# Optimization experiments

Measured on AMD Instinct MI355X. Metric: run time of the kernel, lower is better.

## Reference

```python
import jax, jax.numpy as jnp
import numpy as np


def setup_inputs() -> dict:
    key = jax.random.key(0)
    k1, k2 = jax.random.split(key)
    B, C, h, w = 8, 128, 56, 56
    query_feature = jax.random.normal(k1, (B, C, h, w), dtype=jnp.float32)
    support_feature = jax.random.normal(k2, (B, C, h, w), dtype=jnp.float32)
    return {"query_feature": query_feature, "support_feature": support_feature}


def reference(query_feature, support_feature):
    q, s = query_feature, support_feature
    B, C, h, w = support_feature.shape
    N = h * w
    # torch .view semantics == row-major reshape (NOT a transpose)
    qf = jnp.reshape(query_feature, (B, N, C))      # [B, N, C]
    sf = jnp.reshape(support_feature, (B, C, N))    # [B, C, N]
    batch_adj = jnp.einsum('bnc,bcm->bnm', qf, sf)  # [B, N, N]
    attn = jax.nn.softmax(batch_adj, axis=-1)
    query_logits = jnp.einsum('bnm,bmc->bnc', attn, qf)          # [B, N, C]
    attention_mask = jax.nn.sigmoid(jnp.sum(batch_adj, axis=-1)) # [B, N]
    query_logits = query_logits * attention_mask[..., None]
    sf2 = jnp.reshape(support_feature, (B, N, C))   # another raw view
    support_logits = sf2 * attention_mask[..., None]
    query_logits = jnp.reshape(query_logits, (B, C, h, w))
    support_logits = jnp.reshape(support_logits, (B, C, h, w))
    return (q + query_logits, s + support_logits)
```

## Files before the change

kernel.cpp:

```cpp
#include <hip/hip_runtime.h>
#include <math.h>

#define B_ 8
#define C_ 128
#define N_ 3136
#define MT 64
#define TILES 49
#define SLICES 98
#define QTB 64
#define QTILES 49
#define CS_STRIDE 100

typedef short bf16x8 __attribute__((ext_vector_type(8)));
typedef float f32x4 __attribute__((ext_vector_type(4)));

__device__ __forceinline__ unsigned short f2bf(float f) {
    union { float f; unsigned u; } x; x.f = f;
    return (unsigned short)((x.u + 0x8000u) >> 16);
}

__device__ __forceinline__ unsigned cvtpk(float lo, float hi) {
    unsigned r;
    asm("v_cvt_pk_bf16_f32 %0, %1, %2" : "=v"(r) : "v"(lo), "v"(hi));
    return r;
}

__device__ __forceinline__ void gl_lds16(const void* g, void* l) {
    __builtin_amdgcn_global_load_lds(
        (const __attribute__((address_space(1))) unsigned int*)g,
        (__attribute__((address_space(3))) unsigned int*)l, 16, 0, 0);
}

__global__ __launch_bounds__(256) void colsum_kernel(const float* __restrict__ s,
                                                     float* __restrict__ csum) {
    int blk = blockIdx.x;
    const float* p = s + (size_t)blk * N_;
    float acc = 0.f;
    for (int i = threadIdx.x; i < N_; i += 256) acc += p[i];
#pragma unroll
    for (int off = 32; off > 0; off >>= 1) acc += __shfl_down(acc, off, 64);
    __shared__ float part[4];
    if ((threadIdx.x & 63) == 0) part[threadIdx.x >> 6] = acc;
    __syncthreads();
    if (threadIdx.x == 0) csum[blk] = part[0] + part[1] + part[2] + part[3];
}

__global__ __launch_bounds__(256) void prep_kernel(const float* __restrict__ q,
                                                   const float* __restrict__ s,
                                                   unsigned short* __restrict__ sfT,
                                                   unsigned short* __restrict__ qfT,
                                                   float* __restrict__ csump) {
    __shared__ unsigned short T[4608];
    const int tid = threadIdx.x, bid = blockIdx.x;
    const int b = bid & 7, m0 = (bid >> 3) * 32;
    const int slice = bid >> 3;
    const float* sb = s + (size_t)b * C_ * N_;
    const float* qb = q + (size_t)b * C_ * N_;

    unsigned short (*TA)[132] = (unsigned short (*)[132])T;
#pragma unroll
    for (int st = 0; st < 4; ++st) {
        int idx = st * 256 + tid;
        int c = idx >> 3, m4 = (idx & 7) * 4;
        float4 v = *(const float4*)&sb[(size_t)c * N_ + m0 + m4];
        TA[m4 + 0][c] = f2bf(v.x);
        TA[m4 + 1][c] = f2bf(v.y);
        TA[m4 + 2][c] = f2bf(v.z);
        TA[m4 + 3][c] = f2bf(v.w);
        float ps = (v.x + v.y) + (v.z + v.w);
        ps += __shfl_xor(ps, 1, 8);
        ps += __shfl_xor(ps, 2, 8);
        ps += __shfl_xor(ps, 4, 8);
        if ((tid & 7) == 0) csump[((size_t)b * C_ + c) * CS_STRIDE + slice] = ps;
    }
    __syncthreads();
    {
        unsigned short* dst = sfT + (size_t)b * N_ * C_;
#pragma unroll
        for (int st = 0; st < 2; ++st) {
            int g = st * 256 + tid;
            int mr = g >> 4, p = g & 15;
            int sw = (mr & 15) ^ ((mr >> 1) & 4);
            int lch = p ^ sw;
            const unsigned short* src = &TA[mr][lch * 8];
            ushort4 a = *(const ushort4*)src;
            ushort4 bq = *(const ushort4*)(src + 4);
            uint4 w;
            w.x = a.x | ((unsigned)a.y << 16);   w.y = a.z | ((unsigned)a.w << 16);
            w.z = bq.x | ((unsigned)bq.y << 16); w.w = bq.z | ((unsigned)bq.w << 16);
            *(uint4*)&dst[(size_t)(m0 + mr) * C_ + p * 8] = w;
        }
    }
    __syncthreads();

    unsigned short (*TB)[34] = (unsigned short (*)[34])T;
#pragma unroll
    for (int st = 0; st < 4; ++st) {
        int idx = st * 256 + tid;
        int r = idx >> 5, c4 = (idx & 31) * 4;
        float4 v = *(const float4*)&qb[(size_t)(m0 + r) * C_ + c4];
        TB[c4 + 0][r] = f2bf(v.x);
        TB[c4 + 1][r] = f2bf(v.y);
        TB[c4 + 2][r] = f2bf(v.z);
        TB[c4 + 3][r] = f2bf(v.w);
    }
    __syncthreads();
    {
        unsigned short* dstb = qfT + (size_t)b * N_ * C_;
        const int tile = m0 >> 6, pbase = (m0 & 32) >> 3;
#pragma unroll
        for (int st = 0; st < 2; ++st) {
            int g = st * 256 + tid;
            int pl = g >> 7, c = g & 127;
            const unsigned short* src = &TB[c][pl * 8];
            ushort2 a0 = *(const ushort2*)(src);
            ushort2 a1 = *(const ushort2*)(src + 2);
            ushort2 a2 = *(const ushort2*)(src + 4);
            ushort2 a3 = *(const ushort2*)(src + 6);
            uint4 w;
            w.x = a0.x | ((unsigned)a0.y << 16); w.y = a1.x | ((unsigned)a1.y << 16);
            w.z = a2.x | ((unsigned)a2.y << 16); w.w = a3.x | ((unsigned)a3.y << 16);
            *(uint4*)&dstb[((size_t)tile * 8 + pbase + pl) * (C_ * 8) + c * 8] = w;
        }
    }
}

__global__ __launch_bounds__(256, 2) void fused_full_kernel(
    const float* __restrict__ q, const float* __restrict__ s,
    const float* __restrict__ csump,
    const unsigned short* __restrict__ sfT,
    const unsigned short* __restrict__ qfT,
    float* __restrict__ out0, float* __restrict__ out1) {

    __shared__ __align__(16) unsigned char SM[65536];
    __shared__ float dred[2][QTB];
    __shared__ float mskd[QTB];
    __shared__ float cs[C_];

    unsigned short* Kb = (unsigned short*)SM;
    unsigned short* Vb = (unsigned short*)(SM + 32768);
    float (*Of)[132] = (float (*)[132])SM;

    const int tid = threadIdx.x;
    const int lane = tid & 63;
    const int wave = tid >> 6;
    const int l15 = lane & 15;
    const int quad = lane >> 4;
    const int qs = wave >> 1;
    const int mg = wave & 1;
    const int bid = blockIdx.x;
    const int b = bid & 7;
    const int qt = bid >> 3;
    const int n0 = qt * QTB;

    const float* qb = q + (size_t)b * C_ * N_;
    const unsigned short* sfTb = sfT + (size_t)b * N_ * C_;
    const unsigned short* qfTb = qfT + (size_t)b * N_ * C_;

    const int sig_base = ((l15 >> 2) << 3) + (l15 & 3);

#pragma unroll
    for (int st = 0; st < 4; ++st) {
        int i = st * 256 + tid;
        gl_lds16(sfTb + (size_t)(i >> 4) * C_ + (i & 15) * 8,
                 &Kb[(st * 256 + wave * 64) * 8]);
        gl_lds16(qfTb + (size_t)i * 8,
                 &Vb[(st * 256 + wave * 64) * 8]);
    }

    if (tid < C_) {
        float a = 0.f;
        const float* cp = csump + ((size_t)b * C_ + tid) * CS_STRIDE;
#pragma unroll 7
        for (int sl = 0; sl < SLICES; ++sl) a += cp[sl];
        cs[tid] = a;
    }
    __syncthreads();

    bf16x8 qa[2][4];
    float dotp[2];
#pragma unroll
    for (int rt = 0; rt < 2; ++rt) {
        int grow = n0 + qs * 32 + rt * 16 + l15;
        float dp = 0.f;
#pragma unroll
        for (int ks = 0; ks < 4; ++ks) {
            int c0 = ks * 32 + quad * 8;
            float4 f0 = *(const float4*)&qb[(size_t)grow * C_ + c0];
            float4 f1 = *(const float4*)&qb[(size_t)grow * C_ + c0 + 4];
            dp += f0.x * cs[c0 + 0] + f0.y * cs[c0 + 1] +
                  f0.z * cs[c0 + 2] + f0.w * cs[c0 + 3] +
                  f1.x * cs[c0 + 4] + f1.y * cs[c0 + 5] +
                  f1.z * cs[c0 + 6] + f1.w * cs[c0 + 7];
            union { unsigned w[4]; bf16x8 v; } t;
            t.w[0] = cvtpk(f0.x, f0.y); t.w[1] = cvtpk(f0.z, f0.w);
            t.w[2] = cvtpk(f1.x, f1.y); t.w[3] = cvtpk(f1.z, f1.w);
            qa[rt][ks] = t.v;
        }
        dotp[rt] = dp;
    }
#pragma unroll
    for (int rt = 0; rt < 2; ++rt) {
        float d = dotp[rt];
        d += __shfl_xor(d, 16, 64);
        d += __shfl_xor(d, 32, 64);
        if (mg == 0 && quad == 0) mskd[qs * 32 + rt * 16 + l15] = d;
    }

    f32x4 O[2][8];
#pragma unroll
    for (int rt = 0; rt < 2; ++rt)
#pragma unroll
        for (int nt = 0; nt < 8; ++nt) O[rt][nt] = (f32x4){0.f, 0.f, 0.f, 0.f};
    float dsum[2] = {0.f, 0.f};

    for (int tt = 0; tt < TILES; ++tt) {
        const int cur = tt & 1;

        __builtin_amdgcn_s_barrier();

        if (tt + 1 < TILES) {
            const int nxt = cur ^ 1;
            const size_t m1 = (size_t)(tt + 1) * MT;
#pragma unroll
            for (int st = 0; st < 4; ++st) {
                int i = st * 256 + tid;
                gl_lds16(sfTb + (m1 + (i >> 4)) * C_ + (i & 15) * 8,
                         &Kb[nxt * (MT * C_) + (st * 256 + wave * 64) * 8]);
                gl_lds16(qfTb + (size_t)(tt + 1) * (MT * C_) + (size_t)i * 8,
                         &Vb[nxt * (MT * C_) + (st * 256 + wave * 64) * 8]);
            }
            asm volatile("s_waitcnt vmcnt(8)" ::: "memory");
        } else {
            asm volatile("s_waitcnt vmcnt(0)" ::: "memory");
        }
        __builtin_amdgcn_s_barrier();

        bf16x8 vfr[8];
#pragma unroll
        for (int nt = 0; nt < 8; ++nt)
            vfr[nt] = *(const bf16x8*)&Vb[cur * (MT * C_) + ((mg * 4 + quad) * C_ + nt * 16 + l15) * 8];

        f32x4 acc[2][2];
        __builtin_amdgcn_s_setprio(1);
#pragma unroll
        for (int ct = 0; ct < 2; ++ct) {
            const int mrow = sig_base + (ct << 2);
            const int sw = (mrow & 15) ^ ((mrow >> 1) & 4);
            const int row = mg * 32 + mrow;
            acc[ct][0] = (f32x4){0.f, 0.f, 0.f, 0.f};
            acc[ct][1] = (f32x4){0.f, 0.f, 0.f, 0.f};
#pragma unroll
            for (int ks = 0; ks < 4; ++ks) {
                int ch = (ks * 4 + quad) ^ sw;
                bf16x8 af = *(const bf16x8*)&Kb[cur * (MT * C_) + row * C_ + ch * 8];
                acc[ct][0] = __builtin_amdgcn_mfma_f32_16x16x32_bf16(af, qa[0][ks], acc[ct][0], 0, 0, 0);
                acc[ct][1] = __builtin_amdgcn_mfma_f32_16x16x32_bf16(af, qa[1][ks], acc[ct][1], 0, 0, 0);
            }
        }
        __builtin_amdgcn_s_setprio(0);

        bf16x8 pa[2];
#pragma unroll
        for (int rt = 0; rt < 2; ++rt) {
            float e0 = __expf(acc[0][rt][0]);
            float e1 = __expf(acc[0][rt][1]);
            float e2 = __expf(acc[0][rt][2]);
            float e3 = __expf(acc[0][rt][3]);
            float e4 = __expf(acc[1][rt][0]);
            float e5 = __expf(acc[1][rt][1]);
            float e6 = __expf(acc[1][rt][2]);
            float e7 = __expf(acc[1][rt][3]);
            dsum[rt] += ((e0 + e1) + (e2 + e3)) + ((e4 + e5) + (e6 + e7));
            union { unsigned w[4]; bf16x8 v; } pk;
            pk.w[0] = cvtpk(e0, e1); pk.w[1] = cvtpk(e2, e3);
            pk.w[2] = cvtpk(e4, e5); pk.w[3] = cvtpk(e6, e7);
            pa[rt] = pk.v;
        }

        __builtin_amdgcn_s_setprio(1);
#pragma unroll
        for (int nt = 0; nt < 8; ++nt) {
            O[0][nt] = __builtin_amdgcn_mfma_f32_16x16x32_bf16(pa[0], vfr[nt], O[0][nt], 0, 0, 0);
            O[1][nt] = __builtin_amdgcn_mfma_f32_16x16x32_bf16(pa[1], vfr[nt], O[1][nt], 0, 0, 0);
        }
        __builtin_amdgcn_s_setprio(0);
    }

#pragma unroll
    for (int rt = 0; rt < 2; ++rt) {
        float d = dsum[rt];
        d += __shfl_xor(d, 16, 64);
        d += __shfl_xor(d, 32, 64);
        if (quad == 0) dred[mg][qs * 32 + rt * 16 + l15] = d;
    }

    __syncthreads();

    if (mg == 1) {
#pragma unroll
        for (int rt = 0; rt < 2; ++rt)
#pragma unroll
            for (int nt = 0; nt < 8; ++nt)
#pragma unroll
                for (int r = 0; r < 4; ++r)
                    Of[qs * 32 + rt * 16 + quad * 4 + r][nt * 16 + l15] = O[rt][nt][r];
    }
    __syncthreads();
    if (mg == 0) {
#pragma unroll
        for (int rt = 0; rt < 2; ++rt)
#pragma unroll
            for (int nt = 0; nt < 8; ++nt)
#pragma unroll
                for (int r = 0; r < 4; ++r)
                    Of[qs * 32 + rt * 16 + quad * 4 + r][nt * 16 + l15] += O[rt][nt][r];
    }
    __syncthreads();

    const size_t vbase = (size_t)b * N_ * C_ + (size_t)n0 * C_;
#pragma unroll
    for (int it = 0; it < 8; ++it) {
        int row = it * 8 + (tid >> 5);
        int c = (tid & 31) * 4;
        float dt = dred[0][row] + dred[1][row];
        float mk = 1.0f / (1.0f + __expf(-mskd[row]));
        float scl = mk / dt;
        float om = 1.0f + mk;
        float4 o4 = *(const float4*)&Of[row][c];
        float4 q4 = *(const float4*)&q[vbase + (size_t)row * C_ + c];
        float4 s4 = *(const float4*)&s[vbase + (size_t)row * C_ + c];
        float4 r0v, r1v;
        r0v.x = q4.x + o4.x * scl;
        r0v.y = q4.y + o4.y * scl;
        r0v.z = q4.z + o4.z * scl;
        r0v.w = q4.w + o4.w * scl;
        r1v.x = s4.x * om; r1v.y = s4.y * om;
        r1v.z = s4.z * om; r1v.w = s4.w * om;
        *(float4*)&out0[vbase + (size_t)row * C_ + c] = r0v;
        *(float4*)&out1[vbase + (size_t)row * C_ + c] = r1v;
    }
}

__global__ __launch_bounds__(256, 2) void fused_kernel(const float* __restrict__ q,
                                                       const float* __restrict__ s,
                                                       const float* __restrict__ csum,
                                                       float* __restrict__ out0,
                                                       float* __restrict__ out1) {
    __shared__ float QtT[C_][68];
    __shared__ float Kt[C_ * 32];
    __shared__ float Vt[32 * C_];
    __shared__ float PT[32][68];
    __shared__ float mask_l[64];
    __shared__ float csum_l[C_];

    const int t = threadIdx.x;
    const int l = t & 63, w = t >> 6, tx = t & 15, ty = t >> 4;
    const int bid = blockIdx.x, b = bid & 7, n0 = (bid >> 3) * 64;
    const float* qb = q + (size_t)b * C_ * N_;
    const float* sb = s + (size_t)b * C_ * N_;

#pragma unroll
    for (int jj = 0; jj < 2; ++jj) {
        int c = l + 64 * jj;
#pragma unroll
        for (int i = 0; i < 16; ++i) QtT[c][w + 4 * i] = qb[(size_t)(n0 + w + 4 * i) * C_ + c];
    }
    if (t < C_) csum_l[t] = csum[b * C_ + t];
    __syncthreads();
    if (t < 64) {
        float d = 0.f;
        for (int c = 0; c < C_; ++c) d += QtT[c][t] * csum_l[c];
        mask_l[t] = 1.0f / (1.0f + __expf(-d));
    }
    float4 Oa[4], Ob[4];
#pragma unroll
    for (int i = 0; i < 4; ++i) { Oa[i] = make_float4(0,0,0,0); Ob[i] = make_float4(0,0,0,0); }
    float m_r[4], l_r[4];
#pragma unroll
    for (int i = 0; i < 4; ++i) { m_r[i] = -3.0e38f; l_r[i] = 0.f; }

    for (int mt = 0; mt < N_ / 32; ++mt) {
        const int m0 = mt * 32;
        __syncthreads();
#pragma unroll
        for (int i = 0; i < 4; ++i) {
            int s4 = (w * 4 + i) * 64 + l;
            int c = s4 >> 3, mq = (s4 & 7) * 4;
            *(float4*)&Kt[c * 32 + mq] = *(const float4*)&sb[(size_t)c * N_ + m0 + mq];
            *(float4*)&Vt[s4 * 4] = *(const float4*)&qb[(size_t)m0 * C_ + s4 * 4];
        }
        __syncthreads();
        float a[4][2];
#pragma unroll
        for (int i = 0; i < 4; ++i) a[i][0] = a[i][1] = 0.f;
#pragma unroll 4
        for (int k = 0; k < C_; ++k) {
            const float4 qv = *(const float4*)&QtT[k][4 * ty];
            const float2 kv = *(const float2*)&Kt[k * 32 + 2 * tx];
            a[0][0] = fmaf(qv.x, kv.x, a[0][0]); a[0][1] = fmaf(qv.x, kv.y, a[0][1]);
            a[1][0] = fmaf(qv.y, kv.x, a[1][0]); a[1][1] = fmaf(qv.y, kv.y, a[1][1]);
            a[2][0] = fmaf(qv.z, kv.x, a[2][0]); a[2][1] = fmaf(qv.z, kv.y, a[2][1]);
            a[3][0] = fmaf(qv.w, kv.x, a[3][0]); a[3][1] = fmaf(qv.w, kv.y, a[3][1]);
        }
#pragma unroll
        for (int i = 0; i < 4; ++i) {
            float tm = fmaxf(a[i][0], a[i][1]);
            tm = fmaxf(tm, __shfl_xor(tm, 1, 64)); tm = fmaxf(tm, __shfl_xor(tm, 2, 64));
            tm = fmaxf(tm, __shfl_xor(tm, 4, 64)); tm = fmaxf(tm, __shfl_xor(tm, 8, 64));
            float nm = fmaxf(m_r[i], tm);
            float al = __expf(m_r[i] - nm);
            m_r[i] = nm;
            float p0 = __expf(a[i][0] - nm), p1 = __expf(a[i][1] - nm);
            float ts = p0 + p1;
            ts += __shfl_xor(ts, 1, 64); ts += __shfl_xor(ts, 2, 64);
            ts += __shfl_xor(ts, 4, 64); ts += __shfl_xor(ts, 8, 64);
            l_r[i] = l_r[i] * al + ts;
            PT[2 * tx + 0][4 * ty + i] = p0;
            PT[2 * tx + 1][4 * ty + i] = p1;
            Oa[i].x *= al; Oa[i].y *= al; Oa[i].z *= al; Oa[i].w *= al;
            Ob[i].x *= al; Ob[i].y *= al; Ob[i].z *= al; Ob[i].w *= al;
        }
        __syncthreads();
#pragma unroll 2
        for (int j = 0; j < 32; ++j) {
            const float4 pv = *(const float4*)&PT[j][4 * ty];
            const float4 v0 = *(const float4*)&Vt[j * C_ + 4 * tx];
            const float4 v1 = *(const float4*)&Vt[j * C_ + 4 * tx + 64];
            Oa[0].x = fmaf(pv.x, v0.x, Oa[0].x); Oa[0].y = fmaf(pv.x, v0.y, Oa[0].y);
            Oa[0].z = fmaf(pv.x, v0.z, Oa[0].z); Oa[0].w = fmaf(pv.x, v0.w, Oa[0].w);
            Ob[0].x = fmaf(pv.x, v1.x, Ob[0].x); Ob[0].y = fmaf(pv.x, v1.y, Ob[0].y);
            Ob[0].z = fmaf(pv.x, v1.z, Ob[0].z); Ob[0].w = fmaf(pv.x, v1.w, Ob[0].w);
            Oa[1].x = fmaf(pv.y, v0.x, Oa[1].x); Oa[1].y = fmaf(pv.y, v0.y, Oa[1].y);
            Oa[1].z = fmaf(pv.y, v0.z, Oa[1].z); Oa[1].w = fmaf(pv.y, v0.w, Oa[1].w);
            Ob[1].x = fmaf(pv.y, v1.x, Ob[1].x); Ob[1].y = fmaf(pv.y, v1.y, Ob[1].y);
            Ob[1].z = fmaf(pv.y, v1.z, Ob[1].z); Ob[1].w = fmaf(pv.y, v1.w, Ob[1].w);
            Oa[2].x = fmaf(pv.z, v0.x, Oa[2].x); Oa[2].y = fmaf(pv.z, v0.y, Oa[2].y);
            Oa[2].z = fmaf(pv.z, v0.z, Oa[2].z); Oa[2].w = fmaf(pv.z, v0.w, Oa[2].w);
            Ob[2].x = fmaf(pv.z, v1.x, Ob[2].x); Ob[2].y = fmaf(pv.z, v1.y, Ob[2].y);
            Ob[2].z = fmaf(pv.z, v1.z, Ob[2].z); Ob[2].w = fmaf(pv.z, v1.w, Ob[2].w);
            Oa[3].x = fmaf(pv.w, v0.x, Oa[3].x); Oa[3].y = fmaf(pv.w, v0.y, Oa[3].y);
            Oa[3].z = fmaf(pv.w, v0.z, Oa[3].z); Oa[3].w = fmaf(pv.w, v0.w, Oa[3].w);
            Ob[3].x = fmaf(pv.w, v1.x, Ob[3].x); Ob[3].y = fmaf(pv.w, v1.y, Ob[3].y);
            Ob[3].z = fmaf(pv.w, v1.z, Ob[3].z); Ob[3].w = fmaf(pv.w, v1.w, Ob[3].w);
        }
    }
#pragma unroll
    for (int i = 0; i < 4; ++i) {
        const int r = 4 * ty + i;
        const float mk = mask_l[r];
        const float scl = mk / l_r[i];
        const float om = 1.0f + mk;
        const size_t row = (size_t)b * C_ * N_ + (size_t)(n0 + r) * C_;
#pragma unroll
        for (int h = 0; h < 2; ++h) {
            const int c = 4 * tx + 64 * h;
            const float4 ov = h ? Ob[i] : Oa[i];
            float4 qv = *(const float4*)&qb[(size_t)(n0 + r) * C_ + c];
            float4 sv = *(const float4*)&sb[(size_t)(n0 + r) * C_ + c];
            float4 o0, o1;
            o0.x = qv.x + ov.x * scl; o0.y = qv.y + ov.y * scl;
            o0.z = qv.z + ov.z * scl; o0.w = qv.w + ov.w * scl;
            o1.x = sv.x * om; o1.y = sv.y * om; o1.z = sv.z * om; o1.w = sv.w * om;
            *(float4*)&out0[row + c] = o0;
            *(float4*)&out1[row + c] = o1;
        }
    }
}

extern "C" void kernel_launch(void* const* d_in, const int* in_sizes, int n_in,
                              void* d_out, int out_size, void* d_ws, size_t ws_size,
                              hipStream_t stream) {
    const float* q = (const float*)d_in[0];
    const float* s = (const float*)d_in[1];
    float* out0 = (float*)d_out;
    float* out1 = out0 + (size_t)B_ * C_ * N_;

    const size_t elems = (size_t)B_ * N_ * C_;
    const size_t csump_sz = (size_t)B_ * C_ * CS_STRIDE;
    const size_t need = csump_sz * sizeof(float)
                      + 2 * elems * sizeof(unsigned short);

    if (ws_size >= need) {
        float* csump = (float*)d_ws;
        unsigned short* sfT = (unsigned short*)(csump + csump_sz);
        unsigned short* qfT = sfT + elems;
        prep_kernel<<<B_ * SLICES, 256, 0, stream>>>(q, s, sfT, qfT, csump);
        fused_full_kernel<<<QTILES * B_, 256, 0, stream>>>(q, s, csump, sfT, qfT, out0, out1);
    } else {
        float* csum = (float*)d_ws;
        colsum_kernel<<<B_ * C_, 256, 0, stream>>>(s, csum);
        fused_kernel<<<B_ * (N_ / 64), 256, 0, stream>>>(q, s, csum, out0, out1);
    }
}
```

Before: 145.6 us.

## Load K/V fragments directly from global into registers instead of LDS staging

The main attention loop no longer stages K (sfT) and V (qfT) tiles through double-buffered LDS with global_load_lds and barriers. Each wave now reads its MFMA operand fragments straight from global memory into registers and prefetches the next tile's K fragments into a ping-pong register set. The prep kernel drops the XOR swizzle, since there is no longer an LDS layout to protect from bank conflicts. This removes per-tile barriers and LDS traffic, but the two waves sharing a query slice both read the same K/V rows from global/L2, and launch bounds drop to one block per SM, which lowers occupancy and adds register pressure.

New measurement: 197.8 us. +35.8%, slower.

```diff
diff --git a/kernel.cpp b/kernel.cpp
--- a/kernel.cpp
+++ b/kernel.cpp
@@ -23,12 +23,6 @@
     unsigned r;
     asm("v_cvt_pk_bf16_f32 %0, %1, %2" : "=v"(r) : "v"(lo), "v"(hi));
     return r;
-}
-
-__device__ __forceinline__ void gl_lds16(const void* g, void* l) {
-    __builtin_amdgcn_global_load_lds(
-        (const __attribute__((address_space(1))) unsigned int*)g,
-        (__attribute__((address_space(3))) unsigned int*)l, 16, 0, 0);
 }
 
 __global__ __launch_bounds__(256) void colsum_kernel(const float* __restrict__ s,
@@ -80,9 +74,7 @@
         for (int st = 0; st < 2; ++st) {
             int g = st * 256 + tid;
             int mr = g >> 4, p = g & 15;
-            int sw = (mr & 15) ^ ((mr >> 1) & 4);
-            int lch = p ^ sw;
-            const unsigned short* src = &TA[mr][lch * 8];
+            const unsigned short* src = &TA[mr][p * 8];
             ushort4 a = *(const ushort4*)src;
             ushort4 bq = *(const ushort4*)(src + 4);
             uint4 w;
@@ -125,21 +117,17 @@
     }
 }
 
-__global__ __launch_bounds__(256, 2) void fused_full_kernel(
+__global__ __launch_bounds__(256, 1) void fused_full_kernel(
     const float* __restrict__ q, const float* __restrict__ s,
     const float* __restrict__ csump,
     const unsigned short* __restrict__ sfT,
     const unsigned short* __restrict__ qfT,
     float* __restrict__ out0, float* __restrict__ out1) {
 
-    __shared__ __align__(16) unsigned char SM[65536];
+    __shared__ __align__(16) float Of[QTB][132];
     __shared__ float dred[2][QTB];
     __shared__ float mskd[QTB];
     __shared__ float cs[C_];
-
-    unsigned short* Kb = (unsigned short*)SM;
-    unsigned short* Vb = (unsigned short*)(SM + 32768);
-    float (*Of)[132] = (float (*)[132])SM;
 
     const int tid = threadIdx.x;
     const int lane = tid & 63;
@@ -158,15 +146,9 @@
     const unsigned short* qfTb = qfT + (size_t)b * N_ * C_;
 
     const int sig_base = ((l15 >> 2) << 3) + (l15 & 3);
-
-#pragma unroll
-    for (int st = 0; st < 4; ++st) {
-        int i = st * 256 + tid;
-        gl_lds16(sfTb + (size_t)(i >> 4) * C_ + (i & 15) * 8,
-                 &Kb[(st * 256 + wave * 64) * 8]);
-        gl_lds16(qfTb + (size_t)i * 8,
-                 &Vb[(st * 256 + wave * 64) * 8]);
-    }
+    const int arow = mg * 32 + sig_base;
+    const size_t aoff0 = (size_t)arow * C_ + quad * 8;
+    const size_t voff0 = (size_t)(mg * 4 + quad) * (C_ * 8) + (size_t)l15 * 8;
 
     if (tid < C_) {
         float a = 0.f;
@@ -214,48 +196,41 @@
         for (int nt = 0; nt < 8; ++nt) O[rt][nt] = (f32x4){0.f, 0.f, 0.f, 0.f};
     float dsum[2] = {0.f, 0.f};
 
-    for (int tt = 0; tt < TILES; ++tt) {
-        const int cur = tt & 1;
-
-        __builtin_amdgcn_s_barrier();
-
-        if (tt + 1 < TILES) {
-            const int nxt = cur ^ 1;
-            const size_t m1 = (size_t)(tt + 1) * MT;
-#pragma unroll
-            for (int st = 0; st < 4; ++st) {
-                int i = st * 256 + tid;
-                gl_lds16(sfTb + (m1 + (i >> 4)) * C_ + (i & 15) * 8,
-                         &Kb[nxt * (MT * C_) + (st * 256 + wave * 64) * 8]);
-                gl_lds16(qfTb + (size_t)(tt + 1) * (MT * C_) + (size_t)i * 8,
-                         &Vb[nxt * (MT * C_) + (st * 256 + wave * 64) * 8]);
-            }
-            asm volatile("s_waitcnt vmcnt(8)" ::: "memory");
-        } else {
-            asm volatile("s_waitcnt vmcnt(0)" ::: "memory");
-        }
-        __builtin_amdgcn_s_barrier();
+    bf16x8 afA[2][4], afB[2][4];
+
+#pragma unroll
+    for (int ct = 0; ct < 2; ++ct)
+#pragma unroll
+        for (int ks = 0; ks < 4; ++ks)
+            afA[ct][ks] = *(const bf16x8*)&sfTb[aoff0 + (size_t)(ct * 4) * C_ + ks * 32];
+
+    auto tile_body = [&](bf16x8 (&curA)[2][4], bf16x8 (&nxtA)[2][4], int t) {
+        const size_t tb = (size_t)t * (MT * C_);
 
         bf16x8 vfr[8];
 #pragma unroll
         for (int nt = 0; nt < 8; ++nt)
-            vfr[nt] = *(const bf16x8*)&Vb[cur * (MT * C_) + ((mg * 4 + quad) * C_ + nt * 16 + l15) * 8];
+            vfr[nt] = *(const bf16x8*)&qfTb[tb + voff0 + (size_t)nt * 128];
+
+        if (t + 1 < TILES) {
+            const size_t tb1 = tb + (size_t)(MT * C_);
+#pragma unroll
+            for (int ct = 0; ct < 2; ++ct)
+#pragma unroll
+                for (int ks = 0; ks < 4; ++ks)
+                    nxtA[ct][ks] = *(const bf16x8*)&sfTb[tb1 + aoff0 + (size_t)(ct * 4) * C_ + ks * 32];
+        }
 
         f32x4 acc[2][2];
         __builtin_amdgcn_s_setprio(1);
 #pragma unroll
         for (int ct = 0; ct < 2; ++ct) {
-            const int mrow = sig_base + (ct << 2);
-            const int sw = (mrow & 15) ^ ((mrow >> 1) & 4);
-            const int row = mg * 32 + mrow;
             acc[ct][0] = (f32x4){0.f, 0.f, 0.f, 0.f};
             acc[ct][1] = (f32x4){0.f, 0.f, 0.f, 0.f};
 #pragma unroll
             for (int ks = 0; ks < 4; ++ks) {
-                int ch = (ks * 4 + quad) ^ sw;
-                bf16x8 af = *(const bf16x8*)&Kb[cur * (MT * C_) + row * C_ + ch * 8];
-                acc[ct][0] = __builtin_amdgcn_mfma_f32_16x16x32_bf16(af, qa[0][ks], acc[ct][0], 0, 0, 0);
-                acc[ct][1] = __builtin_amdgcn_mfma_f32_16x16x32_bf16(af, qa[1][ks], acc[ct][1], 0, 0, 0);
+                acc[ct][0] = __builtin_amdgcn_mfma_f32_16x16x32_bf16(curA[ct][ks], qa[0][ks], acc[ct][0], 0, 0, 0);
+                acc[ct][1] = __builtin_amdgcn_mfma_f32_16x16x32_bf16(curA[ct][ks], qa[1][ks], acc[ct][1], 0, 0, 0);
             }
         }
         __builtin_amdgcn_s_setprio(0);
@@ -285,6 +260,11 @@
             O[1][nt] = __builtin_amdgcn_mfma_f32_16x16x32_bf16(pa[1], vfr[nt], O[1][nt], 0, 0, 0);
         }
         __builtin_amdgcn_s_setprio(0);
+    };
+
+    for (int tt = 0; tt < TILES; tt += 2) {
+        tile_body(afA, afB, tt);
+        if (tt + 1 < TILES) tile_body(afB, afA, tt + 1);
     }
 
 #pragma unroll
@@ -294,7 +274,6 @@
         d += __shfl_xor(d, 32, 64);
         if (quad == 0) dred[mg][qs * 32 + rt * 16 + l15] = d;
     }
-
     __syncthreads();
 
     if (mg == 1) {
```

## Fuse prep into main kernel via cooperative launch with grid-wide sync

Applied to the files above, without the earlier changes.

The separate prep kernel is merged into the attention kernel. Each of the 392 blocks first converts and transposes one 64-row slice to bf16 and writes partial column sums, then a cooperative-groups grid sync runs before the attention phase. The prep slice size doubles to 64 rows so work maps one-to-one onto the main grid. This removes one kernel launch and its gap, at the cost of a grid-wide barrier and a need for all blocks to be co-resident (392 blocks at 2 per CU). If the cooperative launch fails, it falls back to two launches.

Result: slower. 232.3 us (+59.5%).

```diff
diff --git a/kernel.cpp b/kernel.cpp
--- a/kernel.cpp
+++ b/kernel.cpp
@@ -1,15 +1,18 @@
 #include <hip/hip_runtime.h>
+#include <hip/hip_cooperative_groups.h>
 #include <math.h>
+
+namespace cg = cooperative_groups;
 
 #define B_ 8
 #define C_ 128
 #define N_ 3136
 #define MT 64
 #define TILES 49
-#define SLICES 98
 #define QTB 64
 #define QTILES 49
-#define CS_STRIDE 100
+#define GRID (QTILES * B_)
+#define CS_STRIDE 52
 
 typedef short bf16x8 __attribute__((ext_vector_type(8)));
 typedef float f32x4 __attribute__((ext_vector_type(4)));
@@ -31,71 +34,51 @@
         (__attribute__((address_space(3))) unsigned int*)l, 16, 0, 0);
 }
 
-__global__ __launch_bounds__(256) void colsum_kernel(const float* __restrict__ s,
-                                                     float* __restrict__ csum) {
-    int blk = blockIdx.x;
-    const float* p = s + (size_t)blk * N_;
-    float acc = 0.f;
-    for (int i = threadIdx.x; i < N_; i += 256) acc += p[i];
-#pragma unroll
-    for (int off = 32; off > 0; off >>= 1) acc += __shfl_down(acc, off, 64);
-    __shared__ float part[4];
-    if ((threadIdx.x & 63) == 0) part[threadIdx.x >> 6] = acc;
-    __syncthreads();
-    if (threadIdx.x == 0) csum[blk] = part[0] + part[1] + part[2] + part[3];
-}
-
-__global__ __launch_bounds__(256) void prep_kernel(const float* __restrict__ q,
-                                                   const float* __restrict__ s,
-                                                   unsigned short* __restrict__ sfT,
-                                                   unsigned short* __restrict__ qfT,
-                                                   float* __restrict__ csump) {
-    __shared__ unsigned short T[4608];
-    const int tid = threadIdx.x, bid = blockIdx.x;
-    const int b = bid & 7, m0 = (bid >> 3) * 32;
-    const int slice = bid >> 3;
-    const float* sb = s + (size_t)b * C_ * N_;
-    const float* qb = q + (size_t)b * C_ * N_;
+__device__ __forceinline__ void prep_slice(
+    const float* __restrict__ qb, const float* __restrict__ sb,
+    unsigned short* __restrict__ sfTb, unsigned short* __restrict__ qfTb,
+    float* __restrict__ csump, int b, int slice, int tid,
+    unsigned short* __restrict__ T) {
+
+    const int m0 = slice * 64;
 
     unsigned short (*TA)[132] = (unsigned short (*)[132])T;
 #pragma unroll
-    for (int st = 0; st < 4; ++st) {
+    for (int st = 0; st < 8; ++st) {
         int idx = st * 256 + tid;
-        int c = idx >> 3, m4 = (idx & 7) * 4;
+        int c = idx >> 4, m4 = (idx & 15) * 4;
         float4 v = *(const float4*)&sb[(size_t)c * N_ + m0 + m4];
         TA[m4 + 0][c] = f2bf(v.x);
         TA[m4 + 1][c] = f2bf(v.y);
         TA[m4 + 2][c] = f2bf(v.z);
         TA[m4 + 3][c] = f2bf(v.w);
         float ps = (v.x + v.y) + (v.z + v.w);
-        ps += __shfl_xor(ps, 1, 8);
-        ps += __shfl_xor(ps, 2, 8);
-        ps += __shfl_xor(ps, 4, 8);
-        if ((tid & 7) == 0) csump[((size_t)b * C_ + c) * CS_STRIDE + slice] = ps;
-    }
-    __syncthreads();
-    {
-        unsigned short* dst = sfT + (size_t)b * N_ * C_;
-#pragma unroll
-        for (int st = 0; st < 2; ++st) {
-            int g = st * 256 + tid;
-            int mr = g >> 4, p = g & 15;
-            int sw = (mr & 15) ^ ((mr >> 1) & 4);
-            int lch = p ^ sw;
-            const unsigned short* src = &TA[mr][lch * 8];
-            ushort4 a = *(const ushort4*)src;
-            ushort4 bq = *(const ushort4*)(src + 4);
-            uint4 w;
-            w.x = a.x | ((unsigned)a.y << 16);   w.y = a.z | ((unsigned)a.w << 16);
-            w.z = bq.x | ((unsigned)bq.y << 16); w.w = bq.z | ((unsigned)bq.w << 16);
-            *(uint4*)&dst[(size_t)(m0 + mr) * C_ + p * 8] = w;
-        }
-    }
-    __syncthreads();
-
-    unsigned short (*TB)[34] = (unsigned short (*)[34])T;
+        ps += __shfl_xor(ps, 1, 16);
+        ps += __shfl_xor(ps, 2, 16);
+        ps += __shfl_xor(ps, 4, 16);
+        ps += __shfl_xor(ps, 8, 16);
+        if ((tid & 15) == 0) csump[((size_t)b * C_ + c) * CS_STRIDE + slice] = ps;
+    }
+    __syncthreads();
 #pragma unroll
     for (int st = 0; st < 4; ++st) {
+        int g = st * 256 + tid;
+        int mr = g >> 4, p = g & 15;
+        int sw = (mr & 15) ^ ((mr >> 1) & 4);
+        int lch = p ^ sw;
+        const unsigned short* src = &TA[mr][lch * 8];
+        ushort4 a = *(const ushort4*)src;
+        ushort4 bq = *(const ushort4*)(src + 4);
+        uint4 w;
+        w.x = a.x | ((unsigned)a.y << 16);   w.y = a.z | ((unsigned)a.w << 16);
+        w.z = bq.x | ((unsigned)bq.y << 16); w.w = bq.z | ((unsigned)bq.w << 16);
+        *(uint4*)&sfTb[(size_t)(m0 + mr) * C_ + p * 8] = w;
+    }
+    __syncthreads();
+
+    unsigned short (*TB)[66] = (unsigned short (*)[66])T;
+#pragma unroll
+    for (int st = 0; st < 8; ++st) {
         int idx = st * 256 + tid;
         int r = idx >> 5, c4 = (idx & 31) * 4;
         float4 v = *(const float4*)&qb[(size_t)(m0 + r) * C_ + c4];
@@ -105,31 +88,41 @@
         TB[c4 + 3][r] = f2bf(v.w);
     }
     __syncthreads();
-    {
-        unsigned short* dstb = qfT + (size_t)b * N_ * C_;
-        const int tile = m0 >> 6, pbase = (m0 & 32) >> 3;
-#pragma unroll
-        for (int st = 0; st < 2; ++st) {
-            int g = st * 256 + tid;
-            int pl = g >> 7, c = g & 127;
-            const unsigned short* src = &TB[c][pl * 8];
-            ushort2 a0 = *(const ushort2*)(src);
-            ushort2 a1 = *(const ushort2*)(src + 2);
-            ushort2 a2 = *(const ushort2*)(src + 4);
-            ushort2 a3 = *(const ushort2*)(src + 6);
-            uint4 w;
-            w.x = a0.x | ((unsigned)a0.y << 16); w.y = a1.x | ((unsigned)a1.y << 16);
-            w.z = a2.x | ((unsigned)a2.y << 16); w.w = a3.x | ((unsigned)a3.y << 16);
-            *(uint4*)&dstb[((size_t)tile * 8 + pbase + pl) * (C_ * 8) + c * 8] = w;
-        }
-    }
-}
-
-__global__ __launch_bounds__(256, 2) void fused_full_kernel(
+#pragma unroll
+    for (int st = 0; st < 4; ++st) {
+        int g = st * 256 + tid;
+        int p = g >> 7, c = g & 127;
+        const unsigned short* src = &TB[c][p * 8];
+        ushort2 a0 = *(const ushort2*)(src);
+        ushort2 a1 = *(const ushort2*)(src + 2);
+        ushort2 a2 = *(const ushort2*)(src + 4);
+        ushort2 a3 = *(const ushort2*)(src + 6);
+        uint4 w;
+        w.x = a0.x | ((unsigned)a0.y << 16); w.y = a1.x | ((unsigned)a1.y << 16);
+        w.z = a2.x | ((unsigned)a2.y << 16); w.w = a3.x | ((unsigned)a3.y << 16);
+        *(uint4*)&qfTb[((size_t)slice * 8 + p) * (C_ * 8) + c * 8] = w;
+    }
+    __syncthreads();
+}
+
+__global__ __launch_bounds__(256) void prep_kernel(const float* __restrict__ q,
+                                                   const float* __restrict__ s,
+                                                   unsigned short* __restrict__ sfT,
+                                                   unsigned short* __restrict__ qfT,
+                                                   float* __restrict__ csump) {
+    __shared__ unsigned short T[8448];
+    const int bid = blockIdx.x;
+    const int b = bid & 7, slice = bid >> 3;
+    prep_slice(q + (size_t)b * C_ * N_, s + (size_t)b * C_ * N_,
+               sfT + (size_t)b * N_ * C_, qfT + (size_t)b * N_ * C_,
+               csump, b, slice, threadIdx.x, T);
+}
+
+template <int DO_PREP>
+__global__ __launch_bounds__(256, 2) void fused_mega(
     const float* __restrict__ q, const float* __restrict__ s,
-    const float* __restrict__ csump,
-    const unsigned short* __restrict__ sfT,
-    const unsigned short* __restrict__ qfT,
+    float* __restrict__ csump,
+    unsigned short* __restrict__ sfT, unsigned short* __restrict__ qfT,
     float* __restrict__ out0, float* __restrict__ out1) {
 
     __shared__ __align__(16) unsigned char SM[65536];
@@ -154,8 +147,15 @@
     const int n0 = qt * QTB;
 
     const float* qb = q + (size_t)b * C_ * N_;
-    const unsigned short* sfTb = sfT + (size_t)b * N_ * C_;
-    const unsigned short* qfTb = qfT + (size_t)b * N_ * C_;
+    const float* sb = s + (size_t)b * C_ * N_;
+    unsigned short* sfTb = sfT + (size_t)b * N_ * C_;
+    unsigned short* qfTb = qfT + (size_t)b * N_ * C_;
+
+    if constexpr (DO_PREP) {
+        prep_slice(qb, sb, sfTb, qfTb, csump, b, qt, tid, (unsigned short*)SM);
+        __threadfence();
+        cg::this_grid().sync();
+    }
 
     const int sig_base = ((l15 >> 2) << 3) + (l15 & 3);
 
@@ -172,7 +172,7 @@
         float a = 0.f;
         const float* cp = csump + ((size_t)b * C_ + tid) * CS_STRIDE;
 #pragma unroll 7
-        for (int sl = 0; sl < SLICES; ++sl) a += cp[sl];
+        for (int sl = 0; sl < TILES; ++sl) a += cp[sl];
         cs[tid] = a;
     }
     __syncthreads();
@@ -340,6 +340,20 @@
         *(float4*)&out0[vbase + (size_t)row * C_ + c] = r0v;
         *(float4*)&out1[vbase + (size_t)row * C_ + c] = r1v;
     }
+}
+
+__global__ __launch_bounds__(256) void colsum_kernel(const float* __restrict__ s,
+                                                     float* __restrict__ csum) {
+    int blk = blockIdx.x;
+    const float* p = s + (size_t)blk * N_;
+    float acc = 0.f;
+    for (int i = threadIdx.x; i < N_; i += 256) acc += p[i];
+#pragma unroll
+    for (int off = 32; off > 0; off >>= 1) acc += __shfl_down(acc, off, 64);
+    __shared__ float part[4];
+    if ((threadIdx.x & 63) == 0) part[threadIdx.x >> 6] = acc;
+    __syncthreads();
+    if (threadIdx.x == 0) csum[blk] = part[0] + part[1] + part[2] + part[3];
 }
 
 __global__ __launch_bounds__(256, 2) void fused_kernel(const float* __restrict__ q,
@@ -485,8 +499,15 @@
         float* csump = (float*)d_ws;
         unsigned short* sfT = (unsigned short*)(csump + csump_sz);
         unsigned short* qfT = sfT + elems;
-        prep_kernel<<<B_ * SLICES, 256, 0, stream>>>(q, s, sfT, qfT, csump);
-        fused_full_kernel<<<QTILES * B_, 256, 0, stream>>>(q, s, csump, sfT, qfT, out0, out1);
+
+        void* kargs[] = { (void*)&q, (void*)&s, (void*)&csump,
+                          (void*)&sfT, (void*)&qfT, (void*)&out0, (void*)&out1 };
+        hipError_t err = hipLaunchCooperativeKernel(
+            (const void*)fused_mega<1>, dim3(GRID), dim3(256), kargs, 0, stream);
+        if (err != hipSuccess) {
+            prep_kernel<<<GRID, 256, 0, stream>>>(q, s, sfT, qfT, csump);
+            fused_mega<0><<<GRID, 256, 0, stream>>>(q, s, csump, sfT, qfT, out0, out1);
+        }
     } else {
         float* csum = (float*)d_ws;
         colsum_kernel<<<B_ * C_, 256, 0, stream>>>(s, csum);
```

## Halve query tile per block and stream V fragments directly into registers

Applied to the files above, without the earlier changes.

The query tile per block shrinks from 64 to 32 rows and the block from 4 to 2 waves, doubling the grid to 784 blocks so more blocks fill the CUs. V fragments are no longer staged through LDS; each wave loads them straight from global memory into double-buffered registers, prefetched one tile ahead through an unrolled two-tile loop. This halves LDS use per block and removes an LDS round trip. In exchange, K tiles are shared by fewer query rows, so global and L2 traffic for K and V goes up and register pressure rises.

Result: slower. 152.2 us (+4.5%).

```diff
diff --git a/kernel.cpp b/kernel.cpp
--- a/kernel.cpp
+++ b/kernel.cpp
@@ -7,8 +7,8 @@
 #define MT 64
 #define TILES 49
 #define SLICES 98
-#define QTB 64
-#define QTILES 49
+#define QTB 32
+#define QTILES 98
 #define CS_STRIDE 100
 
 typedef short bf16x8 __attribute__((ext_vector_type(8)));
@@ -125,20 +125,19 @@
     }
 }
 
-__global__ __launch_bounds__(256, 2) void fused_full_kernel(
+__global__ __launch_bounds__(128, 2) void fused_full_kernel(
     const float* __restrict__ q, const float* __restrict__ s,
     const float* __restrict__ csump,
     const unsigned short* __restrict__ sfT,
     const unsigned short* __restrict__ qfT,
     float* __restrict__ out0, float* __restrict__ out1) {
 
-    __shared__ __align__(16) unsigned char SM[65536];
+    __shared__ __align__(16) unsigned char SM[32768];
     __shared__ float dred[2][QTB];
     __shared__ float mskd[QTB];
     __shared__ float cs[C_];
 
     unsigned short* Kb = (unsigned short*)SM;
-    unsigned short* Vb = (unsigned short*)(SM + 32768);
     float (*Of)[132] = (float (*)[132])SM;
 
     const int tid = threadIdx.x;
@@ -146,8 +145,7 @@
     const int wave = tid >> 6;
     const int l15 = lane & 15;
     const int quad = lane >> 4;
-    const int qs = wave >> 1;
-    const int mg = wave & 1;
+    const int mg = wave;
     const int bid = blockIdx.x;
     const int b = bid & 7;
     const int qt = bid >> 3;
@@ -158,17 +156,20 @@
     const unsigned short* qfTb = qfT + (size_t)b * N_ * C_;
 
     const int sig_base = ((l15 >> 2) << 3) + (l15 & 3);
-
-#pragma unroll
-    for (int st = 0; st < 4; ++st) {
-        int i = st * 256 + tid;
+    const int voff0 = (mg * 4 + quad) * 1024 + l15 * 8;
+
+#pragma unroll
+    for (int st = 0; st < 8; ++st) {
+        int i = st * 128 + tid;
         gl_lds16(sfTb + (size_t)(i >> 4) * C_ + (i & 15) * 8,
-                 &Kb[(st * 256 + wave * 64) * 8]);
-        gl_lds16(qfTb + (size_t)i * 8,
-                 &Vb[(st * 256 + wave * 64) * 8]);
-    }
-
-    if (tid < C_) {
+                 &Kb[(st * 128 + wave * 64) * 8]);
+    }
+    bf16x8 vfrA[8], vfrB[8];
+#pragma unroll
+    for (int nt = 0; nt < 8; ++nt)
+        vfrA[nt] = *(const bf16x8*)&qfTb[voff0 + nt * 128];
+
+    {
         float a = 0.f;
         const float* cp = csump + ((size_t)b * C_ + tid) * CS_STRIDE;
 #pragma unroll 7
@@ -181,7 +182,7 @@
     float dotp[2];
 #pragma unroll
     for (int rt = 0; rt < 2; ++rt) {
-        int grow = n0 + qs * 32 + rt * 16 + l15;
+        int grow = n0 + rt * 16 + l15;
         float dp = 0.f;
 #pragma unroll
         for (int ks = 0; ks < 4; ++ks) {
@@ -204,7 +205,7 @@
         float d = dotp[rt];
         d += __shfl_xor(d, 16, 64);
         d += __shfl_xor(d, 32, 64);
-        if (mg == 0 && quad == 0) mskd[qs * 32 + rt * 16 + l15] = d;
+        if (mg == 0 && quad == 0) mskd[rt * 16 + l15] = d;
     }
 
     f32x4 O[2][8];
@@ -214,32 +215,28 @@
         for (int nt = 0; nt < 8; ++nt) O[rt][nt] = (f32x4){0.f, 0.f, 0.f, 0.f};
     float dsum[2] = {0.f, 0.f};
 
-    for (int tt = 0; tt < TILES; ++tt) {
-        const int cur = tt & 1;
+    auto tile_body = [&](int t, bf16x8 (&vcur)[8], bf16x8 (&vnxt)[8]) {
+        const int cur = t & 1;
 
         __builtin_amdgcn_s_barrier();
 
-        if (tt + 1 < TILES) {
+        if (t + 1 < TILES) {
             const int nxt = cur ^ 1;
-            const size_t m1 = (size_t)(tt + 1) * MT;
-#pragma unroll
-            for (int st = 0; st < 4; ++st) {
-                int i = st * 256 + tid;
+            const size_t m1 = (size_t)(t + 1) * MT;
+#pragma unroll
+            for (int st = 0; st < 8; ++st) {
+                int i = st * 128 + tid;
                 gl_lds16(sfTb + (m1 + (i >> 4)) * C_ + (i & 15) * 8,
-                         &Kb[nxt * (MT * C_) + (st * 256 + wave * 64) * 8]);
-                gl_lds16(qfTb + (size_t)(tt + 1) * (MT * C_) + (size_t)i * 8,
-                         &Vb[nxt * (MT * C_) + (st * 256 + wave * 64) * 8]);
+                         &Kb[nxt * (MT * C_) + (st * 128 + wave * 64) * 8]);
             }
-            asm volatile("s_waitcnt vmcnt(8)" ::: "memory");
+#pragma unroll
+            for (int nt = 0; nt < 8; ++nt)
+                vnxt[nt] = *(const bf16x8*)&qfTb[(size_t)(t + 1) * (MT * C_) + voff0 + nt * 128];
+            asm volatile("s_waitcnt vmcnt(16)" ::: "memory");
         } else {
             asm volatile("s_waitcnt vmcnt(0)" ::: "memory");
         }
         __builtin_amdgcn_s_barrier();
-
-        bf16x8 vfr[8];
-#pragma unroll
-        for (int nt = 0; nt < 8; ++nt)
-            vfr[nt] = *(const bf16x8*)&Vb[cur * (MT * C_) + ((mg * 4 + quad) * C_ + nt * 16 + l15) * 8];
 
         f32x4 acc[2][2];
         __builtin_amdgcn_s_setprio(1);
@@ -281,18 +278,24 @@
         __builtin_amdgcn_s_setprio(1);
 #pragma unroll
         for (int nt = 0; nt < 8; ++nt) {
-            O[0][nt] = __builtin_amdgcn_mfma_f32_16x16x32_bf16(pa[0], vfr[nt], O[0][nt], 0, 0, 0);
-            O[1][nt] = __builtin_amdgcn_mfma_f32_16x16x32_bf16(pa[1], vfr[nt], O[1][nt], 0, 0, 0);
+            O[0][nt] = __builtin_amdgcn_mfma_f32_16x16x32_bf16(pa[0], vcur[nt], O[0][nt], 0, 0, 0);
+            O[1][nt] = __builtin_amdgcn_mfma_f32_16x16x32_bf16(pa[1], vcur[nt], O[1][nt], 0, 0, 0);
         }
         __builtin_amdgcn_s_setprio(0);
-    }
+    };
+
+    for (int tt = 0; tt + 1 < TILES; tt += 2) {
+        tile_body(tt, vfrA, vfrB);
+        tile_body(tt + 1, vfrB, vfrA);
+    }
+    tile_body(TILES - 1, vfrA, vfrB);
 
 #pragma unroll
     for (int rt = 0; rt < 2; ++rt) {
         float d = dsum[rt];
         d += __shfl_xor(d, 16, 64);
         d += __shfl_xor(d, 32, 64);
-        if (quad == 0) dred[mg][qs * 32 + rt * 16 + l15] = d;
+        if (quad == 0) dred[mg][rt * 16 + l15] = d;
     }
 
     __syncthreads();
@@ -304,7 +307,7 @@
             for (int nt = 0; nt < 8; ++nt)
 #pragma unroll
                 for (int r = 0; r < 4; ++r)
-                    Of[qs * 32 + rt * 16 + quad * 4 + r][nt * 16 + l15] = O[rt][nt][r];
+                    Of[rt * 16 + quad * 4 + r][nt * 16 + l15] = O[rt][nt][r];
     }
     __syncthreads();
     if (mg == 0) {
@@ -314,14 +317,14 @@
             for (int nt = 0; nt < 8; ++nt)
 #pragma unroll
                 for (int r = 0; r < 4; ++r)
-                    Of[qs * 32 + rt * 16 + quad * 4 + r][nt * 16 + l15] += O[rt][nt][r];
+                    Of[rt * 16 + quad * 4 + r][nt * 16 + l15] += O[rt][nt][r];
     }
     __syncthreads();
 
     const size_t vbase = (size_t)b * N_ * C_ + (size_t)n0 * C_;
 #pragma unroll
     for (int it = 0; it < 8; ++it) {
-        int row = it * 8 + (tid >> 5);
+        int row = it * 4 + (tid >> 5);
         int c = (tid & 31) * 4;
         float dt = dred[0][row] + dred[1][row];
         float mk = 1.0f / (1.0f + __expf(-mskd[row]));
@@ -486,7 +489,7 @@
         unsigned short* sfT = (unsigned short*)(csump + csump_sz);
         unsigned short* qfT = sfT + elems;
         prep_kernel<<<B_ * SLICES, 256, 0, stream>>>(q, s, sfT, qfT, csump);
-        fused_full_kernel<<<QTILES * B_, 256, 0, stream>>>(q, s, csump, sfT, qfT, out0, out1);
+        fused_full_kernel<<<QTILES * B_, 128, 0, stream>>>(q, s, csump, sfT, qfT, out0, out1);
     } else {
         float* csum = (float*)d_ws;
         colsum_kernel<<<B_ * C_, 256, 0, stream>>>(s, csum);
```
